# Performance work log

Measured on AMD Instinct MI355X. Metric: run time of the kernel, lower is better.

Reference implementation:

```python
import jax, jax.numpy as jnp
import numpy as np

IN_C = 256
ATTN_C = IN_C // 8
B, H, W = 4, 64, 64


def setup_inputs() -> dict:
    key = jax.random.key(0)
    ks = jax.random.split(key, 8)
    x = jax.random.normal(ks[0], (B, IN_C, W, H), dtype=jnp.float32)
    # 1x1 convs == channel-mixing matmuls: weight [out_c, in_c], bias [out_c]
    sq = 1.0 / np.sqrt(IN_C)
    Wq = jax.random.normal(ks[1], (ATTN_C, IN_C), dtype=jnp.float32) * sq
    bq = jnp.zeros((ATTN_C,), dtype=jnp.float32)
    Wk = jax.random.normal(ks[2], (ATTN_C, IN_C), dtype=jnp.float32) * sq
    bk = jnp.zeros((ATTN_C,), dtype=jnp.float32)
    Wv = jax.random.normal(ks[3], (IN_C, IN_C), dtype=jnp.float32) * sq
    bv = jnp.zeros((IN_C,), dtype=jnp.float32)
    # gamma initialized to zeros in the torch module; use a nonzero value so
    # the attention path contributes to the output/gradients.
    gamma = jnp.full((1,), 0.5, dtype=jnp.float32)
    return {"x": x, "Wq": Wq, "bq": bq, "Wk": Wk, "bk": bk,
            "Wv": Wv, "bv": bv, "gamma": gamma}


def reference(x, Wq, bq, Wk, bk, Wv, bv, gamma):
    bs, c, w, h = x.shape
    n = w * h
    xf = x.reshape(bs, c, n)                                   # [B, C, N]
    q = jnp.einsum('ac,bcn->ban', Wq, xf) + bq[:, None]        # [B, A, N]
    k = jnp.einsum('ac,bcn->ban', Wk, xf) + bk[:, None]        # [B, A, N]
    v = jnp.einsum('oc,bcn->bon', Wv, xf) + bv[:, None]        # [B, C, N]
    # energy = query.transpose(1,2) @ key  -> energy[b,i,j] = sum_a q[b,a,i] k[b,a,j]
    energy = jnp.einsum('bai,baj->bij', q, k)                  # [B, N, N]
    # non-standard: softmax over dim=1 (the query/i axis)
    attn = jax.nn.softmax(energy, axis=1)
    # out = value @ attn.transpose(1,2) -> out[b,c,i] = sum_j v[b,c,j] attn[b,i,j]
    out = jnp.einsum('bcj,bij->bci', v, attn)                  # [B, C, N]
    out = out.reshape(bs, c, w, h)
    return gamma * out + x
```

## Files before the change

kernel.cpp:

```cpp
#include <hip/hip_runtime.h>

#define NBATCH 4
#define CIN 256
#define CATT 32
#define NPIX 4096

static constexpr float LOG2E_F = 1.4426950408889634f;

typedef __attribute__((ext_vector_type(8))) short bf16x8;
typedef __attribute__((ext_vector_type(4))) float f32x4;

__device__ __forceinline__ unsigned short f2bf_rne(float f) {
    unsigned u = __builtin_bit_cast(unsigned, f);
    return (unsigned short)((u + 0x7fffu + ((u >> 16) & 1u)) >> 16);
}

__global__ __launch_bounds__(256, 2)
void proj_qk_kernel(const float* __restrict__ Wq, const float* __restrict__ bq,
                    const float* __restrict__ Wk, const float* __restrict__ bk,
                    const float* __restrict__ x,
                    unsigned short* __restrict__ qt, unsigned short* __restrict__ kt)
{
    __shared__ float sWq[32][33];
    __shared__ float sWk[32][33];
    __shared__ float sX[32][128];
    const int t = threadIdx.x;
    const int nblk = blockIdx.x * 128;
    const int b = blockIdx.y;
    const float* xb = x + (size_t)b * CIN * NPIX;
    const int tx = t & 31, ty = t >> 5;
    float aq[4][4] = {}, ak[4][4] = {};

    for (int c0 = 0; c0 < CIN; c0 += 32) {
        __syncthreads();
        {
            const int r = t >> 3, c4 = (t & 7) << 2;
            float4 w4 = *reinterpret_cast<const float4*>(&Wq[(size_t)r * CIN + c0 + c4]);
            sWq[r][c4] = w4.x; sWq[r][c4+1] = w4.y; sWq[r][c4+2] = w4.z; sWq[r][c4+3] = w4.w;
            w4 = *reinterpret_cast<const float4*>(&Wk[(size_t)r * CIN + c0 + c4]);
            sWk[r][c4] = w4.x; sWk[r][c4+1] = w4.y; sWk[r][c4+2] = w4.z; sWk[r][c4+3] = w4.w;
        }
        #pragma unroll
        for (int rr = 0; rr < 4; ++rr) {
            const int r = (t >> 5) + (rr << 3);
            const int c4 = (t & 31) << 2;
            *reinterpret_cast<float4*>(&sX[r][c4]) =
                *reinterpret_cast<const float4*>(&xb[(size_t)(c0 + r) * NPIX + nblk + c4]);
        }
        __syncthreads();
        #pragma unroll
        for (int kk = 0; kk < 32; ++kk) {
            float wq[4], wk[4];
            #pragma unroll
            for (int oo = 0; oo < 4; ++oo) { wq[oo] = sWq[(ty << 2) + oo][kk]; wk[oo] = sWk[(ty << 2) + oo][kk]; }
            const float4 xx = *reinterpret_cast<const float4*>(&sX[kk][tx << 2]);
            const float xv[4] = {xx.x, xx.y, xx.z, xx.w};
            #pragma unroll
            for (int oo = 0; oo < 4; ++oo)
                #pragma unroll
                for (int nn = 0; nn < 4; ++nn) {
                    aq[oo][nn] = fmaf(wq[oo], xv[nn], aq[oo][nn]);
                    ak[oo][nn] = fmaf(wk[oo], xv[nn], ak[oo][nn]);
                }
        }
    }
    float bqv[4], bkv[4];
    #pragma unroll
    for (int oo = 0; oo < 4; ++oo) { bqv[oo] = bq[(ty << 2) + oo]; bkv[oo] = bk[(ty << 2) + oo]; }
    #pragma unroll
    for (int nn = 0; nn < 4; ++nn) {
        const int n = nblk + (tx << 2) + nn;
        ushort4 uq, uk;
        uq.x = f2bf_rne(LOG2E_F * (aq[0][nn] + bqv[0]));
        uq.y = f2bf_rne(LOG2E_F * (aq[1][nn] + bqv[1]));
        uq.z = f2bf_rne(LOG2E_F * (aq[2][nn] + bqv[2]));
        uq.w = f2bf_rne(LOG2E_F * (aq[3][nn] + bqv[3]));
        uk.x = f2bf_rne(ak[0][nn] + bkv[0]);
        uk.y = f2bf_rne(ak[1][nn] + bkv[1]);
        uk.z = f2bf_rne(ak[2][nn] + bkv[2]);
        uk.w = f2bf_rne(ak[3][nn] + bkv[3]);
        const size_t base = ((size_t)b * NPIX + n) * CATT + (ty << 2);
        *reinterpret_cast<ushort4*>(&qt[base]) = uq;
        *reinterpret_cast<ushort4*>(&kt[base]) = uk;
    }
}

__global__ __launch_bounds__(256, 2)
void stats_kernel(const unsigned short* __restrict__ qt,
                  const unsigned short* __restrict__ kt, float* __restrict__ rs)
{
    __shared__ float sred[4][16];
    const int n = blockIdx.x;
    const int b = n & 3;
    const int jblk = (n >> 2) * 32;
    const int t = threadIdx.x, w = t >> 6, l = t & 63, lr = l & 15, lg = l >> 4;
    const int jsl = w & 1;
    const int ih = w >> 1;
    const unsigned short* qb = qt + (size_t)b * NPIX * CATT;
    const unsigned short* kb = kt + (size_t)b * NPIX * CATT;

    const bf16x8 kfrag = *reinterpret_cast<const bf16x8*>(
        &kb[(size_t)(jblk + 16 * jsl + lr) * CATT + lg * 8]);
    const f32x4 zero = {0.f, 0.f, 0.f, 0.f};
    const unsigned short* qp = qb + (size_t)(ih * 2048 + lr) * CATT + lg * 8;

    float s0 = 0.f, s1 = 0.f, s2 = 0.f, s3 = 0.f;
    bf16x8 qc0 = *reinterpret_cast<const bf16x8*>(qp);
    bf16x8 qc1 = *reinterpret_cast<const bf16x8*>(qp + 16 * CATT);
    bf16x8 qc2 = *reinterpret_cast<const bf16x8*>(qp + 32 * CATT);
    bf16x8 qc3 = *reinterpret_cast<const bf16x8*>(qp + 48 * CATT);

    for (int ib = 0; ib < 2048; ib += 64) {
        bf16x8 qn0, qn1, qn2, qn3;
        const bool more = (ib + 64) < 2048;
        if (more) {
            const unsigned short* q2 = qp + (size_t)(ib + 64) * CATT;
            qn0 = *reinterpret_cast<const bf16x8*>(q2);
            qn1 = *reinterpret_cast<const bf16x8*>(q2 + 16 * CATT);
            qn2 = *reinterpret_cast<const bf16x8*>(q2 + 32 * CATT);
            qn3 = *reinterpret_cast<const bf16x8*>(q2 + 48 * CATT);
        }
        f32x4 d;
        d = __builtin_amdgcn_mfma_f32_16x16x32_bf16(kfrag, qc0, zero, 0, 0, 0);
        s0 += __builtin_amdgcn_exp2f(d[0]); s1 += __builtin_amdgcn_exp2f(d[1]);
        s2 += __builtin_amdgcn_exp2f(d[2]); s3 += __builtin_amdgcn_exp2f(d[3]);
        d = __builtin_amdgcn_mfma_f32_16x16x32_bf16(kfrag, qc1, zero, 0, 0, 0);
        s0 += __builtin_amdgcn_exp2f(d[0]); s1 += __builtin_amdgcn_exp2f(d[1]);
        s2 += __builtin_amdgcn_exp2f(d[2]); s3 += __builtin_amdgcn_exp2f(d[3]);
        d = __builtin_amdgcn_mfma_f32_16x16x32_bf16(kfrag, qc2, zero, 0, 0, 0);
        s0 += __builtin_amdgcn_exp2f(d[0]); s1 += __builtin_amdgcn_exp2f(d[1]);
        s2 += __builtin_amdgcn_exp2f(d[2]); s3 += __builtin_amdgcn_exp2f(d[3]);
        d = __builtin_amdgcn_mfma_f32_16x16x32_bf16(kfrag, qc3, zero, 0, 0, 0);
        s0 += __builtin_amdgcn_exp2f(d[0]); s1 += __builtin_amdgcn_exp2f(d[1]);
        s2 += __builtin_amdgcn_exp2f(d[2]); s3 += __builtin_amdgcn_exp2f(d[3]);
        if (more) { qc0 = qn0; qc1 = qn1; qc2 = qn2; qc3 = qn3; }
    }
    #pragma unroll
    for (int m = 1; m < 16; m <<= 1) {
        s0 += __shfl_xor(s0, m); s1 += __shfl_xor(s1, m);
        s2 += __shfl_xor(s2, m); s3 += __shfl_xor(s3, m);
    }
    if (lr == 0) {
        sred[w][(lg << 2) + 0] = s0;
        sred[w][(lg << 2) + 1] = s1;
        sred[w][(lg << 2) + 2] = s2;
        sred[w][(lg << 2) + 3] = s3;
    }
    __syncthreads();
    if (t < 32) {
        const int j16 = t & 15, js = t >> 4;
        const float s = sred[js][j16] + sred[js + 2][j16];
        rs[(size_t)b * NPIX + jblk + t] = 1.0f / s;
    }
}

__global__ __launch_bounds__(256, 2)
void proj_v_kernel(const float* __restrict__ Wv, const float* __restrict__ bv,
                   const float* __restrict__ x, const float* __restrict__ rs,
                   const float* __restrict__ gamma, unsigned short* __restrict__ vt)
{
    __shared__ float sW[32][33];
    __shared__ float sX[32][128];
    const int t = threadIdx.x;
    const int nblk = blockIdx.x * 128;
    const int oblk = blockIdx.y * 32;
    const int b = blockIdx.z;
    const float* xb = x + (size_t)b * CIN * NPIX;
    const int tx = t & 31, ty = t >> 5;
    float acc[4][4] = {};

    for (int c0 = 0; c0 < CIN; c0 += 32) {
        __syncthreads();
        {
            const int r = t >> 3, c4 = (t & 7) << 2;
            const float4 w4 = *reinterpret_cast<const float4*>(&Wv[(size_t)(oblk + r) * CIN + c0 + c4]);
            sW[r][c4] = w4.x; sW[r][c4+1] = w4.y; sW[r][c4+2] = w4.z; sW[r][c4+3] = w4.w;
        }
        #pragma unroll
        for (int rr = 0; rr < 4; ++rr) {
            const int r = (t >> 5) + (rr << 3);
            const int c4 = (t & 31) << 2;
            *reinterpret_cast<float4*>(&sX[r][c4]) =
                *reinterpret_cast<const float4*>(&xb[(size_t)(c0 + r) * NPIX + nblk + c4]);
        }
        __syncthreads();
        #pragma unroll
        for (int kk = 0; kk < 32; ++kk) {
            float wv[4];
            #pragma unroll
            for (int oo = 0; oo < 4; ++oo) wv[oo] = sW[(ty << 2) + oo][kk];
            const float4 xx = *reinterpret_cast<const float4*>(&sX[kk][tx << 2]);
            const float xv[4] = {xx.x, xx.y, xx.z, xx.w};
            #pragma unroll
            for (int oo = 0; oo < 4; ++oo)
                #pragma unroll
                for (int nn = 0; nn < 4; ++nn)
                    acc[oo][nn] = fmaf(wv[oo], xv[nn], acc[oo][nn]);
        }
    }
    const float gv = gamma[0];
    const float4 rs4 = *reinterpret_cast<const float4*>(&rs[(size_t)b * NPIX + nblk + (tx << 2)]);
    #pragma unroll
    for (int oo = 0; oo < 4; ++oo) {
        const int c = oblk + (ty << 2) + oo;
        const float bb = bv[c];
        ushort4 u;
        u.x = f2bf_rne(gv * rs4.x * (acc[oo][0] + bb));
        u.y = f2bf_rne(gv * rs4.y * (acc[oo][1] + bb));
        u.z = f2bf_rne(gv * rs4.z * (acc[oo][2] + bb));
        u.w = f2bf_rne(gv * rs4.w * (acc[oo][3] + bb));
        *reinterpret_cast<ushort4*>(&vt[((size_t)b * CIN + c) * NPIX + nblk + (tx << 2)]) = u;
    }
}

__global__ __launch_bounds__(256, 2)
void out_kernel(const unsigned short* __restrict__ qt,
                const unsigned short* __restrict__ kt,
                const unsigned short* __restrict__ vt,
                const float* __restrict__ x, float* __restrict__ out)
{
    __shared__ unsigned short sP[2][64 * 64];
    const int n = blockIdx.x;
    const int b = n & 3;
    const int rest = n >> 2;
    const int ch = rest & 1;
    const int it = rest >> 1;
    const int iblk = it * 64;
    const int cblk = ch * 128;
    const int t = threadIdx.x, w = t >> 6, l = t & 63, lr = l & 15, lg = l >> 4;
    const unsigned short* qb = qt + (size_t)b * NPIX * CATT;
    const unsigned short* kb = kt + (size_t)b * NPIX * CATT;
    const unsigned short* vb = vt + (size_t)b * CIN * NPIX;
    const f32x4 zero = {0.f, 0.f, 0.f, 0.f};

    bf16x8 qfrag[4];
    #pragma unroll
    for (int nt = 0; nt < 4; ++nt)
        qfrag[nt] = *reinterpret_cast<const bf16x8*>(
            &qb[(size_t)(iblk + 16 * nt + lr) * CATT + lg * 8]);

    const unsigned short* kp = kb + (size_t)(16 * w + lr) * CATT + lg * 8;
    const unsigned short* vp = vb + (size_t)(cblk + 32 * w + lr) * NPIX + lg * 8;

    const int swz = (lr & 7) << 4;
    const int wb0 = lr * 128 + (((16 * w + 4 * lg) * 2) ^ swz);
    const int rb_col0 = (0 * 64 + 16 * lg) ^ swz;
    const int rb_col1 = (1 * 64 + 16 * lg) ^ swz;

    f32x4 acc[2][4] = {};

    bf16x8 kf   = *reinterpret_cast<const bf16x8*>(kp);
    bf16x8 vf00 = *reinterpret_cast<const bf16x8*>(vp);
    bf16x8 vf01 = *reinterpret_cast<const bf16x8*>(vp + 32);
    bf16x8 vf10 = *reinterpret_cast<const bf16x8*>(vp + 16 * (size_t)NPIX);
    bf16x8 vf11 = *reinterpret_cast<const bf16x8*>(vp + 16 * (size_t)NPIX + 32);

    for (int jb = 0; jb < NPIX / 64; ++jb) {
        bf16x8 kf_n, vn00, vn01, vn10, vn11;
        const bool more = jb < NPIX / 64 - 1;
        if (more) {
            const unsigned short* kp2 = kp + (size_t)(jb + 1) * 64 * CATT;
            const unsigned short* vp2 = vp + (size_t)(jb + 1) * 64;
            kf_n = *reinterpret_cast<const bf16x8*>(kp2);
            vn00 = *reinterpret_cast<const bf16x8*>(vp2);
            vn01 = *reinterpret_cast<const bf16x8*>(vp2 + 32);
            vn10 = *reinterpret_cast<const bf16x8*>(vp2 + 16 * (size_t)NPIX);
            vn11 = *reinterpret_cast<const bf16x8*>(vp2 + 16 * (size_t)NPIX + 32);
        }
        char* sp = reinterpret_cast<char*>(&sP[jb & 1][0]);
        #pragma unroll
        for (int nt = 0; nt < 4; ++nt) {
            const f32x4 e = __builtin_amdgcn_mfma_f32_16x16x32_bf16(kf, qfrag[nt], zero, 0, 0, 0);
            const float p0 = __builtin_amdgcn_exp2f(e[0]);
            const float p1 = __builtin_amdgcn_exp2f(e[1]);
            const float p2 = __builtin_amdgcn_exp2f(e[2]);
            const float p3 = __builtin_amdgcn_exp2f(e[3]);
            unsigned w0, w1;
            asm("v_cvt_pk_bf16_f32 %0, %1, %2" : "=v"(w0) : "v"(p0), "v"(p1));
            asm("v_cvt_pk_bf16_f32 %0, %1, %2" : "=v"(w1) : "v"(p2), "v"(p3));
            *reinterpret_cast<uint2*>(sp + wb0 + nt * 2048) = make_uint2(w0, w1);
        }
        __syncthreads();
        #pragma unroll
        for (int kk = 0; kk < 2; ++kk) {
            const int rbc = (kk == 0) ? rb_col0 : rb_col1;
            bf16x8 pf[4];
            #pragma unroll
            for (int nt = 0; nt < 4; ++nt)
                pf[nt] = *reinterpret_cast<const bf16x8*>(sp + lr * 128 + nt * 2048 + rbc);
            __builtin_amdgcn_s_setprio(1);
            #pragma unroll
            for (int nt = 0; nt < 4; ++nt) {
                acc[0][nt] = __builtin_amdgcn_mfma_f32_16x16x32_bf16(
                    kk == 0 ? vf00 : vf01, pf[nt], acc[0][nt], 0, 0, 0);
                acc[1][nt] = __builtin_amdgcn_mfma_f32_16x16x32_bf16(
                    kk == 0 ? vf10 : vf11, pf[nt], acc[1][nt], 0, 0, 0);
            }
            __builtin_amdgcn_s_setprio(0);
        }
        if (more) { kf = kf_n; vf00 = vn00; vf01 = vn01; vf10 = vn10; vf11 = vn11; }
    }

    const float* xb = x + (size_t)b * CIN * NPIX;
    float* ob = out + (size_t)b * CIN * NPIX;
    #pragma unroll
    for (int mt = 0; mt < 2; ++mt)
        #pragma unroll
        for (int nt = 0; nt < 4; ++nt)
            #pragma unroll
            for (int r = 0; r < 4; ++r) {
                const int c = cblk + 32 * w + 16 * mt + (lg << 2) + r;
                const size_t idx = (size_t)c * NPIX + iblk + 16 * nt + lr;
                ob[idx] = acc[mt][nt][r] + xb[idx];
            }
}

extern "C" void kernel_launch(void* const* d_in, const int* in_sizes, int n_in,
                              void* d_out, int out_size, void* d_ws, size_t ws_size,
                              hipStream_t stream)
{
    const float* x     = (const float*)d_in[0];
    const float* Wq    = (const float*)d_in[1];
    const float* bq    = (const float*)d_in[2];
    const float* Wk    = (const float*)d_in[3];
    const float* bk    = (const float*)d_in[4];
    const float* Wv    = (const float*)d_in[5];
    const float* bv    = (const float*)d_in[6];
    const float* gamma = (const float*)d_in[7];
    float* out = (float*)d_out;

    unsigned short* qt = (unsigned short*)d_ws;
    unsigned short* kt = qt + (size_t)NBATCH * NPIX * CATT;
    unsigned short* vt = kt + (size_t)NBATCH * NPIX * CATT;
    float* rsw = (float*)(vt + (size_t)NBATCH * CIN * NPIX);

    proj_qk_kernel<<<dim3(NPIX / 128, NBATCH), 256, 0, stream>>>(Wq, bq, Wk, bk, x, qt, kt);
    stats_kernel<<<dim3((NPIX / 32) * NBATCH), 256, 0, stream>>>(qt, kt, rsw);
    proj_v_kernel<<<dim3(NPIX / 128, CIN / 32, NBATCH), 256, 0, stream>>>(Wv, bv, x, rsw, gamma, vt);
    out_kernel<<<dim3((NPIX / 64) * 2 * NBATCH), 256, 0, stream>>>(qt, kt, vt, x, out);
}
```

Before: 148.3 us.

## Use bf16 MFMA for Q/K/V projections via transposed x and pipeline out_kernel

Adds a transpose kernel that converts x to a bf16 pixel-major layout, then rewrites the QK and V projection kernels to use 16x16x32 bf16 MFMA instead of scalar FP32 FMA loops. Q/K weights are split into hi/lo bf16 pairs to keep precision while V uses plain bf16. The attention output kernel is software-pipelined so that the exp of the next block's scores is interleaved with the PV MFMAs of the current block, with prefetch two blocks ahead. This adds an extra kernel launch and workspace traffic and lowers the precision of the projections.

```diff
diff --git a/kernel.cpp b/kernel.cpp
--- a/kernel.cpp
+++ b/kernel.cpp
@@ -14,72 +14,101 @@
     unsigned u = __builtin_bit_cast(unsigned, f);
     return (unsigned short)((u + 0x7fffu + ((u >> 16) & 1u)) >> 16);
 }
+__device__ __forceinline__ float bf2f(unsigned short h) {
+    unsigned u = (unsigned)h << 16;
+    return __builtin_bit_cast(float, u);
+}
+__device__ __forceinline__ void split8(const float* p, bf16x8& hi, bf16x8& lo) {
+    const float4 a = *reinterpret_cast<const float4*>(p);
+    const float4 b = *reinterpret_cast<const float4*>(p + 4);
+    const float f[8] = {a.x, a.y, a.z, a.w, b.x, b.y, b.z, b.w};
+    #pragma unroll
+    for (int e = 0; e < 8; ++e) {
+        const unsigned short h = f2bf_rne(f[e]);
+        hi[e] = (short)h;
+        lo[e] = (short)f2bf_rne(f[e] - bf2f(h));
+    }
+}
+__device__ __forceinline__ bf16x8 cvt8(const float* p) {
+    const float4 a = *reinterpret_cast<const float4*>(p);
+    const float4 b = *reinterpret_cast<const float4*>(p + 4);
+    const float f[8] = {a.x, a.y, a.z, a.w, b.x, b.y, b.z, b.w};
+    bf16x8 r;
+    #pragma unroll
+    for (int e = 0; e < 8; ++e) r[e] = (short)f2bf_rne(f[e]);
+    return r;
+}
+
+__global__ __launch_bounds__(256, 2)
+void transpose_kernel(const float* __restrict__ x, unsigned short* __restrict__ xT)
+{
+    __shared__ unsigned short sT[64][68];
+    const int t = threadIdx.x;
+    const int nblk = blockIdx.x * 64;
+    const int cblk = blockIdx.y * 64;
+    const int b = blockIdx.z;
+    const float* xb = x + ((size_t)b * CIN + cblk) * NPIX + nblk;
+    const int lc = t >> 2, ln = (t & 3) << 4;
+    #pragma unroll
+    for (int u = 0; u < 4; ++u) {
+        const float4 v = *reinterpret_cast<const float4*>(&xb[(size_t)lc * NPIX + ln + 4 * u]);
+        sT[ln + 4 * u + 0][lc] = f2bf_rne(v.x);
+        sT[ln + 4 * u + 1][lc] = f2bf_rne(v.y);
+        sT[ln + 4 * u + 2][lc] = f2bf_rne(v.z);
+        sT[ln + 4 * u + 3][lc] = f2bf_rne(v.w);
+    }
+    __syncthreads();
+    const int rn = t >> 2, cs = (t & 3) << 4;
+    const uint2 d0 = *reinterpret_cast<const uint2*>(&sT[rn][cs + 0]);
+    const uint2 d1 = *reinterpret_cast<const uint2*>(&sT[rn][cs + 4]);
+    const uint2 d2 = *reinterpret_cast<const uint2*>(&sT[rn][cs + 8]);
+    const uint2 d3 = *reinterpret_cast<const uint2*>(&sT[rn][cs + 12]);
+    unsigned short* dst = xT + ((size_t)b * NPIX + nblk + rn) * CIN + cblk + cs;
+    *reinterpret_cast<uint4*>(dst)     = make_uint4(d0.x, d0.y, d1.x, d1.y);
+    *reinterpret_cast<uint4*>(dst + 8) = make_uint4(d2.x, d2.y, d3.x, d3.y);
+}
 
 __global__ __launch_bounds__(256, 2)
 void proj_qk_kernel(const float* __restrict__ Wq, const float* __restrict__ bq,
                     const float* __restrict__ Wk, const float* __restrict__ bk,
-                    const float* __restrict__ x,
+                    const unsigned short* __restrict__ xT,
                     unsigned short* __restrict__ qt, unsigned short* __restrict__ kt)
 {
-    __shared__ float sWq[32][33];
-    __shared__ float sWk[32][33];
-    __shared__ float sX[32][128];
-    const int t = threadIdx.x;
-    const int nblk = blockIdx.x * 128;
+    const int t = threadIdx.x, w = t >> 6, l = t & 63, lr = l & 15, lg = l >> 4;
     const int b = blockIdx.y;
-    const float* xb = x + (size_t)b * CIN * NPIX;
-    const int tx = t & 31, ty = t >> 5;
-    float aq[4][4] = {}, ak[4][4] = {};
-
-    for (int c0 = 0; c0 < CIN; c0 += 32) {
-        __syncthreads();
-        {
-            const int r = t >> 3, c4 = (t & 7) << 2;
-            float4 w4 = *reinterpret_cast<const float4*>(&Wq[(size_t)r * CIN + c0 + c4]);
-            sWq[r][c4] = w4.x; sWq[r][c4+1] = w4.y; sWq[r][c4+2] = w4.z; sWq[r][c4+3] = w4.w;
-            w4 = *reinterpret_cast<const float4*>(&Wk[(size_t)r * CIN + c0 + c4]);
-            sWk[r][c4] = w4.x; sWk[r][c4+1] = w4.y; sWk[r][c4+2] = w4.z; sWk[r][c4+3] = w4.w;
-        }
-        #pragma unroll
-        for (int rr = 0; rr < 4; ++rr) {
-            const int r = (t >> 5) + (rr << 3);
-            const int c4 = (t & 31) << 2;
-            *reinterpret_cast<float4*>(&sX[r][c4]) =
-                *reinterpret_cast<const float4*>(&xb[(size_t)(c0 + r) * NPIX + nblk + c4]);
-        }
-        __syncthreads();
-        #pragma unroll
-        for (int kk = 0; kk < 32; ++kk) {
-            float wq[4], wk[4];
-            #pragma unroll
-            for (int oo = 0; oo < 4; ++oo) { wq[oo] = sWq[(ty << 2) + oo][kk]; wk[oo] = sWk[(ty << 2) + oo][kk]; }
-            const float4 xx = *reinterpret_cast<const float4*>(&sX[kk][tx << 2]);
-            const float xv[4] = {xx.x, xx.y, xx.z, xx.w};
-            #pragma unroll
-            for (int oo = 0; oo < 4; ++oo)
-                #pragma unroll
-                for (int nn = 0; nn < 4; ++nn) {
-                    aq[oo][nn] = fmaf(wq[oo], xv[nn], aq[oo][nn]);
-                    ak[oo][nn] = fmaf(wk[oo], xv[nn], ak[oo][nn]);
-                }
-        }
-    }
-    float bqv[4], bkv[4];
-    #pragma unroll
-    for (int oo = 0; oo < 4; ++oo) { bqv[oo] = bq[(ty << 2) + oo]; bkv[oo] = bk[(ty << 2) + oo]; }
-    #pragma unroll
-    for (int nn = 0; nn < 4; ++nn) {
-        const int n = nblk + (tx << 2) + nn;
+    const int n0 = blockIdx.x * 64 + 16 * w;
+    const unsigned short* xrow = xT + ((size_t)b * NPIX + n0 + lr) * CIN + lg * 8;
+    f32x4 aq[2] = {{0.f,0.f,0.f,0.f},{0.f,0.f,0.f,0.f}};
+    f32x4 ak2[2] = {{0.f,0.f,0.f,0.f},{0.f,0.f,0.f,0.f}};
+    #pragma unroll
+    for (int ks = 0; ks < 8; ++ks) {
+        const int ko = ks * 32 + lg * 8;
+        const bf16x8 bx = *reinterpret_cast<const bf16x8*>(xrow + ks * 32);
+        #pragma unroll
+        for (int mt = 0; mt < 2; ++mt) {
+            bf16x8 wh, wl;
+            split8(&Wq[(size_t)(mt * 16 + lr) * CIN + ko], wh, wl);
+            aq[mt] = __builtin_amdgcn_mfma_f32_16x16x32_bf16(wh, bx, aq[mt], 0, 0, 0);
+            aq[mt] = __builtin_amdgcn_mfma_f32_16x16x32_bf16(wl, bx, aq[mt], 0, 0, 0);
+            split8(&Wk[(size_t)(mt * 16 + lr) * CIN + ko], wh, wl);
+            ak2[mt] = __builtin_amdgcn_mfma_f32_16x16x32_bf16(wh, bx, ak2[mt], 0, 0, 0);
+            ak2[mt] = __builtin_amdgcn_mfma_f32_16x16x32_bf16(wl, bx, ak2[mt], 0, 0, 0);
+        }
+    }
+    #pragma unroll
+    for (int mt = 0; mt < 2; ++mt) {
+        const float4 b4q = *reinterpret_cast<const float4*>(&bq[16 * mt + (lg << 2)]);
+        const float4 b4k = *reinterpret_cast<const float4*>(&bk[16 * mt + (lg << 2)]);
         ushort4 uq, uk;
-        uq.x = f2bf_rne(LOG2E_F * (aq[0][nn] + bqv[0]));
-        uq.y = f2bf_rne(LOG2E_F * (aq[1][nn] + bqv[1]));
-        uq.z = f2bf_rne(LOG2E_F * (aq[2][nn] + bqv[2]));
-        uq.w = f2bf_rne(LOG2E_F * (aq[3][nn] + bqv[3]));
-        uk.x = f2bf_rne(ak[0][nn] + bkv[0]);
-        uk.y = f2bf_rne(ak[1][nn] + bkv[1]);
-        uk.z = f2bf_rne(ak[2][nn] + bkv[2]);
-        uk.w = f2bf_rne(ak[3][nn] + bkv[3]);
-        const size_t base = ((size_t)b * NPIX + n) * CATT + (ty << 2);
+        uq.x = f2bf_rne(LOG2E_F * (aq[mt][0] + b4q.x));
+        uq.y = f2bf_rne(LOG2E_F * (aq[mt][1] + b4q.y));
+        uq.z = f2bf_rne(LOG2E_F * (aq[mt][2] + b4q.z));
+        uq.w = f2bf_rne(LOG2E_F * (aq[mt][3] + b4q.w));
+        uk.x = f2bf_rne(ak2[mt][0] + b4k.x);
+        uk.y = f2bf_rne(ak2[mt][1] + b4k.y);
+        uk.z = f2bf_rne(ak2[mt][2] + b4k.z);
+        uk.w = f2bf_rne(ak2[mt][3] + b4k.w);
+        const size_t base = ((size_t)b * NPIX + n0 + lr) * CATT + 16 * mt + (lg << 2);
         *reinterpret_cast<ushort4*>(&qt[base]) = uq;
         *reinterpret_cast<ushort4*>(&kt[base]) = uk;
     }
@@ -156,60 +185,46 @@
 
 __global__ __launch_bounds__(256, 2)
 void proj_v_kernel(const float* __restrict__ Wv, const float* __restrict__ bv,
-                   const float* __restrict__ x, const float* __restrict__ rs,
+                   const unsigned short* __restrict__ xT, const float* __restrict__ rs,
                    const float* __restrict__ gamma, unsigned short* __restrict__ vt)
 {
-    __shared__ float sW[32][33];
-    __shared__ float sX[32][128];
-    const int t = threadIdx.x;
-    const int nblk = blockIdx.x * 128;
-    const int oblk = blockIdx.y * 32;
-    const int b = blockIdx.z;
-    const float* xb = x + (size_t)b * CIN * NPIX;
-    const int tx = t & 31, ty = t >> 5;
-    float acc[4][4] = {};
-
-    for (int c0 = 0; c0 < CIN; c0 += 32) {
-        __syncthreads();
-        {
-            const int r = t >> 3, c4 = (t & 7) << 2;
-            const float4 w4 = *reinterpret_cast<const float4*>(&Wv[(size_t)(oblk + r) * CIN + c0 + c4]);
-            sW[r][c4] = w4.x; sW[r][c4+1] = w4.y; sW[r][c4+2] = w4.z; sW[r][c4+3] = w4.w;
-        }
-        #pragma unroll
-        for (int rr = 0; rr < 4; ++rr) {
-            const int r = (t >> 5) + (rr << 3);
-            const int c4 = (t & 31) << 2;
-            *reinterpret_cast<float4*>(&sX[r][c4]) =
-                *reinterpret_cast<const float4*>(&xb[(size_t)(c0 + r) * NPIX + nblk + c4]);
-        }
-        __syncthreads();
-        #pragma unroll
-        for (int kk = 0; kk < 32; ++kk) {
-            float wv[4];
+    const int t = threadIdx.x, w = t >> 6, l = t & 63, lr = l & 15, lg = l >> 4;
+    const int b = blockIdx.y;
+    const int n0 = blockIdx.x * 32;
+    const int cb = 64 * w;
+    const unsigned short* xa = xT + ((size_t)b * NPIX + n0) * CIN;
+    f32x4 acc[2][4] = {};
+    #pragma unroll
+    for (int ks = 0; ks < 8; ++ks) {
+        const int ko = ks * 32 + lg * 8;
+        bf16x8 af[2];
+        #pragma unroll
+        for (int mt = 0; mt < 2; ++mt)
+            af[mt] = *reinterpret_cast<const bf16x8*>(&xa[(size_t)(16 * mt + lr) * CIN + ko]);
+        #pragma unroll
+        for (int ct = 0; ct < 4; ++ct) {
+            const bf16x8 wf = cvt8(&Wv[(size_t)(cb + 16 * ct + lr) * CIN + ko]);
             #pragma unroll
-            for (int oo = 0; oo < 4; ++oo) wv[oo] = sW[(ty << 2) + oo][kk];
-            const float4 xx = *reinterpret_cast<const float4*>(&sX[kk][tx << 2]);
-            const float xv[4] = {xx.x, xx.y, xx.z, xx.w};
-            #pragma unroll
-            for (int oo = 0; oo < 4; ++oo)
-                #pragma unroll
-                for (int nn = 0; nn < 4; ++nn)
-                    acc[oo][nn] = fmaf(wv[oo], xv[nn], acc[oo][nn]);
+            for (int mt = 0; mt < 2; ++mt)
+                acc[mt][ct] = __builtin_amdgcn_mfma_f32_16x16x32_bf16(af[mt], wf, acc[mt][ct], 0, 0, 0);
         }
     }
     const float gv = gamma[0];
-    const float4 rs4 = *reinterpret_cast<const float4*>(&rs[(size_t)b * NPIX + nblk + (tx << 2)]);
-    #pragma unroll
-    for (int oo = 0; oo < 4; ++oo) {
-        const int c = oblk + (ty << 2) + oo;
-        const float bb = bv[c];
-        ushort4 u;
-        u.x = f2bf_rne(gv * rs4.x * (acc[oo][0] + bb));
-        u.y = f2bf_rne(gv * rs4.y * (acc[oo][1] + bb));
-        u.z = f2bf_rne(gv * rs4.z * (acc[oo][2] + bb));
-        u.w = f2bf_rne(gv * rs4.w * (acc[oo][3] + bb));
-        *reinterpret_cast<ushort4*>(&vt[((size_t)b * CIN + c) * NPIX + nblk + (tx << 2)]) = u;
+    #pragma unroll
+    for (int mt = 0; mt < 2; ++mt) {
+        const int nr = n0 + 16 * mt + (lg << 2);
+        const float4 rs4 = *reinterpret_cast<const float4*>(&rs[(size_t)b * NPIX + nr]);
+        #pragma unroll
+        for (int ct = 0; ct < 4; ++ct) {
+            const int c = cb + 16 * ct + lr;
+            const float bb = bv[c];
+            ushort4 u;
+            u.x = f2bf_rne(gv * rs4.x * (acc[mt][ct][0] + bb));
+            u.y = f2bf_rne(gv * rs4.y * (acc[mt][ct][1] + bb));
+            u.z = f2bf_rne(gv * rs4.z * (acc[mt][ct][2] + bb));
+            u.w = f2bf_rne(gv * rs4.w * (acc[mt][ct][3] + bb));
+            *reinterpret_cast<ushort4*>(&vt[((size_t)b * CIN + c) * NPIX + nr]) = u;
+        }
     }
 }
 
@@ -244,33 +259,26 @@
 
     const int swz = (lr & 7) << 4;
     const int wb0 = lr * 128 + (((16 * w + 4 * lg) * 2) ^ swz);
-    const int rb_col0 = (0 * 64 + 16 * lg) ^ swz;
-    const int rb_col1 = (1 * 64 + 16 * lg) ^ swz;
+    const int rb_col0 = (16 * lg) ^ swz;
+    const int rb_col1 = (64 + 16 * lg) ^ swz;
 
     f32x4 acc[2][4] = {};
 
-    bf16x8 kf   = *reinterpret_cast<const bf16x8*>(kp);
-    bf16x8 vf00 = *reinterpret_cast<const bf16x8*>(vp);
-    bf16x8 vf01 = *reinterpret_cast<const bf16x8*>(vp + 32);
-    bf16x8 vf10 = *reinterpret_cast<const bf16x8*>(vp + 16 * (size_t)NPIX);
-    bf16x8 vf11 = *reinterpret_cast<const bf16x8*>(vp + 16 * (size_t)NPIX + 32);
-
-    for (int jb = 0; jb < NPIX / 64; ++jb) {
-        bf16x8 kf_n, vn00, vn01, vn10, vn11;
-        const bool more = jb < NPIX / 64 - 1;
-        if (more) {
-            const unsigned short* kp2 = kp + (size_t)(jb + 1) * 64 * CATT;
-            const unsigned short* vp2 = vp + (size_t)(jb + 1) * 64;
-            kf_n = *reinterpret_cast<const bf16x8*>(kp2);
-            vn00 = *reinterpret_cast<const bf16x8*>(vp2);
-            vn01 = *reinterpret_cast<const bf16x8*>(vp2 + 32);
-            vn10 = *reinterpret_cast<const bf16x8*>(vp2 + 16 * (size_t)NPIX);
-            vn11 = *reinterpret_cast<const bf16x8*>(vp2 + 16 * (size_t)NPIX + 32);
-        }
-        char* sp = reinterpret_cast<char*>(&sP[jb & 1][0]);
+    const bf16x8 kf0 = *reinterpret_cast<const bf16x8*>(kp);
+    bf16x8 vc00 = *reinterpret_cast<const bf16x8*>(vp);
+    bf16x8 vc01 = *reinterpret_cast<const bf16x8*>(vp + 32);
+    bf16x8 vc10 = *reinterpret_cast<const bf16x8*>(vp + 16 * (size_t)NPIX);
+    bf16x8 vc11 = *reinterpret_cast<const bf16x8*>(vp + 16 * (size_t)NPIX + 32);
+    bf16x8 kfA  = *reinterpret_cast<const bf16x8*>(kp + (size_t)64 * CATT);
+    bf16x8 vn00 = *reinterpret_cast<const bf16x8*>(vp + 64);
+    bf16x8 vn01 = *reinterpret_cast<const bf16x8*>(vp + 64 + 32);
+    bf16x8 vn10 = *reinterpret_cast<const bf16x8*>(vp + 16 * (size_t)NPIX + 64);
+    bf16x8 vn11 = *reinterpret_cast<const bf16x8*>(vp + 16 * (size_t)NPIX + 64 + 32);
+    {
+        char* spw = reinterpret_cast<char*>(&sP[0][0]);
         #pragma unroll
         for (int nt = 0; nt < 4; ++nt) {
-            const f32x4 e = __builtin_amdgcn_mfma_f32_16x16x32_bf16(kf, qfrag[nt], zero, 0, 0, 0);
+            const f32x4 e = __builtin_amdgcn_mfma_f32_16x16x32_bf16(kf0, qfrag[nt], zero, 0, 0, 0);
             const float p0 = __builtin_amdgcn_exp2f(e[0]);
             const float p1 = __builtin_amdgcn_exp2f(e[1]);
             const float p2 = __builtin_amdgcn_exp2f(e[2]);
@@ -278,27 +286,96 @@
             unsigned w0, w1;
             asm("v_cvt_pk_bf16_f32 %0, %1, %2" : "=v"(w0) : "v"(p0), "v"(p1));
             asm("v_cvt_pk_bf16_f32 %0, %1, %2" : "=v"(w1) : "v"(p2), "v"(p3));
-            *reinterpret_cast<uint2*>(sp + wb0 + nt * 2048) = make_uint2(w0, w1);
+            *reinterpret_cast<uint2*>(spw + wb0 + nt * 2048) = make_uint2(w0, w1);
+        }
+    }
+    __syncthreads();
+
+    for (int jb = 0; jb < 63; ++jb) {
+        const int jpre = (jb + 2 < 64) ? jb + 2 : 63;
+        const bf16x8 kfN  = *reinterpret_cast<const bf16x8*>(kp + (size_t)jpre * 64 * CATT);
+        const unsigned short* vpp = vp + (size_t)jpre * 64;
+        const bf16x8 vN00 = *reinterpret_cast<const bf16x8*>(vpp);
+        const bf16x8 vN01 = *reinterpret_cast<const bf16x8*>(vpp + 32);
+        const bf16x8 vN10 = *reinterpret_cast<const bf16x8*>(vpp + 16 * (size_t)NPIX);
+        const bf16x8 vN11 = *reinterpret_cast<const bf16x8*>(vpp + 16 * (size_t)NPIX + 32);
+
+        char* spw = reinterpret_cast<char*>(&sP[(jb + 1) & 1][0]);
+        char* spr = reinterpret_cast<char*>(&sP[jb & 1][0]);
+
+        f32x4 e[4];
+        #pragma unroll
+        for (int nt = 0; nt < 4; ++nt)
+            e[nt] = __builtin_amdgcn_mfma_f32_16x16x32_bf16(kfA, qfrag[nt], zero, 0, 0, 0);
+
+        bf16x8 pf[4];
+        #pragma unroll
+        for (int nt = 0; nt < 4; ++nt)
+            pf[nt] = *reinterpret_cast<const bf16x8*>(spr + lr * 128 + nt * 2048 + rb_col0);
+        __builtin_amdgcn_s_setprio(1);
+        #pragma unroll
+        for (int nt = 0; nt < 4; ++nt) {
+            acc[0][nt] = __builtin_amdgcn_mfma_f32_16x16x32_bf16(vc00, pf[nt], acc[0][nt], 0, 0, 0);
+            acc[1][nt] = __builtin_amdgcn_mfma_f32_16x16x32_bf16(vc10, pf[nt], acc[1][nt], 0, 0, 0);
+        }
+        __builtin_amdgcn_s_setprio(0);
+        #pragma unroll
+        for (int h = 0; h < 2; ++h) {
+            const float p0 = __builtin_amdgcn_exp2f(e[h][0]);
+            const float p1 = __builtin_amdgcn_exp2f(e[h][1]);
+            const float p2 = __builtin_amdgcn_exp2f(e[h][2]);
+            const float p3 = __builtin_amdgcn_exp2f(e[h][3]);
+            unsigned w0, w1;
+            asm("v_cvt_pk_bf16_f32 %0, %1, %2" : "=v"(w0) : "v"(p0), "v"(p1));
+            asm("v_cvt_pk_bf16_f32 %0, %1, %2" : "=v"(w1) : "v"(p2), "v"(p3));
+            *reinterpret_cast<uint2*>(spw + wb0 + h * 2048) = make_uint2(w0, w1);
+        }
+        #pragma unroll
+        for (int nt = 0; nt < 4; ++nt)
+            pf[nt] = *reinterpret_cast<const bf16x8*>(spr + lr * 128 + nt * 2048 + rb_col1);
+        __builtin_amdgcn_s_setprio(1);
+        #pragma unroll
+        for (int nt = 0; nt < 4; ++nt) {
+            acc[0][nt] = __builtin_amdgcn_mfma_f32_16x16x32_bf16(vc01, pf[nt], acc[0][nt], 0, 0, 0);
+            acc[1][nt] = __builtin_amdgcn_mfma_f32_16x16x32_bf16(vc11, pf[nt], acc[1][nt], 0, 0, 0);
+        }
+        __builtin_amdgcn_s_setprio(0);
+        #pragma unroll
+        for (int h = 2; h < 4; ++h) {
+            const float p0 = __builtin_amdgcn_exp2f(e[h][0]);
+            const float p1 = __builtin_amdgcn_exp2f(e[h][1]);
+            const float p2 = __builtin_amdgcn_exp2f(e[h][2]);
+            const float p3 = __builtin_amdgcn_exp2f(e[h][3]);
+            unsigned w0, w1;
+            asm("v_cvt_pk_bf16_f32 %0, %1, %2" : "=v"(w0) : "v"(p0), "v"(p1));
+            asm("v_cvt_pk_bf16_f32 %0, %1, %2" : "=v"(w1) : "v"(p2), "v"(p3));
+            *reinterpret_cast<uint2*>(spw + wb0 + h * 2048) = make_uint2(w0, w1);
         }
         __syncthreads();
-        #pragma unroll
-        for (int kk = 0; kk < 2; ++kk) {
-            const int rbc = (kk == 0) ? rb_col0 : rb_col1;
-            bf16x8 pf[4];
-            #pragma unroll
-            for (int nt = 0; nt < 4; ++nt)
-                pf[nt] = *reinterpret_cast<const bf16x8*>(sp + lr * 128 + nt * 2048 + rbc);
-            __builtin_amdgcn_s_setprio(1);
-            #pragma unroll
-            for (int nt = 0; nt < 4; ++nt) {
-                acc[0][nt] = __builtin_amdgcn_mfma_f32_16x16x32_bf16(
-                    kk == 0 ? vf00 : vf01, pf[nt], acc[0][nt], 0, 0, 0);
-                acc[1][nt] = __builtin_amdgcn_mfma_f32_16x16x32_bf16(
-                    kk == 0 ? vf10 : vf11, pf[nt], acc[1][nt], 0, 0, 0);
-            }
-            __builtin_amdgcn_s_setprio(0);
-        }
-        if (more) { kf = kf_n; vf00 = vn00; vf01 = vn01; vf10 = vn10; vf11 = vn11; }
+        kfA = kfN;
+        vc00 = vn00; vc01 = vn01; vc10 = vn10; vc11 = vn11;
+        vn00 = vN00; vn01 = vN01; vn10 = vN10; vn11 = vN11;
+    }
+
+    {
+        char* spr = reinterpret_cast<char*>(&sP[1][0]);
+        bf16x8 pf[4];
+        #pragma unroll
+        for (int nt = 0; nt < 4; ++nt)
+            pf[nt] = *reinterpret_cast<const bf16x8*>(spr + lr * 128 + nt * 2048 + rb_col0);
+        #pragma unroll
+        for (int nt = 0; nt < 4; ++nt) {
+            acc[0][nt] = __builtin_amdgcn_mfma_f32_16x16x32_bf16(vc00, pf[nt], acc[0][nt], 0, 0, 0);
+            acc[1][nt] = __builtin_amdgcn_mfma_f32_16x16x32_bf16(vc10, pf[nt], acc[1][nt], 0, 0, 0);
+        }
+        #pragma unroll
+        for (int nt = 0; nt < 4; ++nt)
+            pf[nt] = *reinterpret_cast<const bf16x8*>(spr + lr * 128 + nt * 2048 + rb_col1);
+        #pragma unroll
+        for (int nt = 0; nt < 4; ++nt) {
+            acc[0][nt] = __builtin_amdgcn_mfma_f32_16x16x32_bf16(vc01, pf[nt], acc[0][nt], 0, 0, 0);
+            acc[1][nt] = __builtin_amdgcn_mfma_f32_16x16x32_bf16(vc11, pf[nt], acc[1][nt], 0, 0, 0);
+        }
     }
 
     const float* xb = x + (size_t)b * CIN * NPIX;
@@ -329,13 +406,15 @@
     const float* gamma = (const float*)d_in[7];
     float* out = (float*)d_out;
 
-    unsigned short* qt = (unsigned short*)d_ws;
+    unsigned short* xT = (unsigned short*)d_ws;
+    unsigned short* qt = xT + (size_t)NBATCH * NPIX * CIN;
     unsigned short* kt = qt + (size_t)NBATCH * NPIX * CATT;
     unsigned short* vt = kt + (size_t)NBATCH * NPIX * CATT;
     float* rsw = (float*)(vt + (size_t)NBATCH * CIN * NPIX);
 
-    proj_qk_kernel<<<dim3(NPIX / 128, NBATCH), 256, 0, stream>>>(Wq, bq, Wk, bk, x, qt, kt);
+    transpose_kernel<<<dim3(NPIX / 64, CIN / 64, NBATCH), 256, 0, stream>>>(x, xT);
+    proj_qk_kernel<<<dim3(NPIX / 64, NBATCH), 256, 0, stream>>>(Wq, bq, Wk, bk, xT, qt, kt);
     stats_kernel<<<dim3((NPIX / 32) * NBATCH), 256, 0, stream>>>(qt, kt, rsw);
-    proj_v_kernel<<<dim3(NPIX / 128, CIN / 32, NBATCH), 256, 0, stream>>>(Wv, bv, x, rsw, gamma, vt);
+    proj_v_kernel<<<dim3(NPIX / 32, NBATCH), 256, 0, stream>>>(Wv, bv, xT, rsw, gamma, vt);
     out_kernel<<<dim3((NPIX / 64) * 2 * NBATCH), 256, 0, stream>>>(qt, kt, vt, x, out);
 }
```

Result: faster. 134.2 us (-9.5%).
